# Optimization experiments

Hardware: AMD Instinct MI355X
Metric: run time of the kernel (lower is better)

Reference implementation:

```python
import jax, jax.numpy as jnp
import numpy as np

N_ATOMS = 50000
N_EDGES = 800000
EMB = 128      # emb_size_atom
EMB_BF = 128   # emb_size_bf
N_HIDDEN = 3
INV_SQRT2 = 0.7071067811865476
SILU_SCALE = 1.0 / 0.6  # GemNet ScaledSiLU


def scaled_silu(x):
    return jax.nn.silu(x) * SILU_SCALE


def residual_layer(x, w0, w1):
    # ResidualLayer(units, nLayers=2): two bias-free Dense+ScaledSiLU, then inv_sqrt(2)*(x + y)
    y = scaled_silu(x @ w0)
    y = scaled_silu(y @ w1)
    return (x + y) * INV_SQRT2


def setup_inputs() -> dict:
    key = jax.random.key(0)
    ks = jax.random.split(key, 9)
    s_emb = 1.0 / np.float32(np.sqrt(EMB))
    s_bf = 1.0 / np.float32(np.sqrt(EMB_BF))
    return {
        "h": jax.random.normal(ks[0], (N_ATOMS, EMB), jnp.float32),
        "bf": jax.random.uniform(ks[1], (N_EDGES, EMB_BF), jnp.float32),
        "idx_s": jax.random.randint(ks[2], (N_EDGES,), 0, N_ATOMS, jnp.int64),
        "idx_t": jax.random.randint(ks[3], (N_EDGES,), 0, N_ATOMS, jnp.int64),
        "w_bf": jax.random.normal(ks[4], (EMB_BF, EMB), jnp.float32) * s_bf,
        "w_pre": jax.random.normal(ks[5], (2, EMB, EMB), jnp.float32) * s_emb,
        "w_mlp1": jax.random.normal(ks[6], (EMB, EMB), jnp.float32) * s_emb,
        "w_res": jax.random.normal(ks[7], (N_HIDDEN, 2, EMB, EMB), jnp.float32) * s_emb,
        "scale_sum": jnp.ones((1,), jnp.float32),  # ScalingFactor (1.0 without scale_file)
    }


def reference(h, bf, idx_s, idx_t, w_bf, w_pre, w_mlp1, w_res, scale_sum):
    # pre_residual
    h_res = residual_layer(h, w_pre[0], w_pre[1])          # (nAtoms, EMB)
    # dense_bf: bias-free linear, no activation
    mlp_bf = bf @ w_bf                                     # (nEdges, EMB)
    # gather source embeddings, Hadamard multiply with edge features
    x = h_res[idx_s] * mlp_bf                              # (nEdges, EMB)
    # scatter-sum over target atoms
    x2 = jax.ops.segment_sum(x, idx_t, num_segments=N_ATOMS)  # (nAtoms, EMB)
    x = x2 * scale_sum[0]
    # MLP: Dense+activation, then nHidden residual blocks
    x = scaled_silu(x @ w_mlp1)
    for i in range(N_HIDDEN):
        x = residual_layer(x, w_res[i, 0], w_res[i, 1])
    return x
```

## Files before the change

kernel.cpp:

```cpp
#include <hip/hip_runtime.h>

#define EMB 128
#define NATOMS 50000
#define NEDGES 800000
#define PADN 50176

typedef __attribute__((ext_vector_type(8))) short bf16x8;
typedef __attribute__((ext_vector_type(4))) float f32x4;

static const size_t H_RES_OFF  = 0;
static const size_t X2_OFF     = (size_t)NATOMS * EMB * 4;
static const size_t W_OFF      = 2 * (size_t)NATOMS * EMB * 4;
static const size_t FLAG_OFF   = W_OFF + 10 * 128 * 128 * 2;
static const size_t COUNTS_OFF = (FLAG_OFF + 4 + 255) & ~(size_t)255;
static const size_t SEG_OFF    = COUNTS_OFF + (size_t)PADN * 4;
static const size_t CURSOR_OFF = SEG_OFF + (size_t)PADN * 4;
static const size_t BSUM_OFF   = CURSOR_OFF + (size_t)PADN * 4;
static const size_t ORDER_OFF  = BSUM_OFF + 1024;

__device__ __forceinline__ short f2bf(float f) {
  unsigned u = __float_as_uint(f);
  u += 0x7fffu + ((u >> 16) & 1u);
  return (short)(u >> 16);
}

__device__ __forceinline__ float ssilu(float x) {
  return x * (1.0f / 0.6f) / (1.0f + __expf(-x));
}

__device__ __forceinline__ int xidx(int row, int k) {
  return (row << 7) + ((((k >> 2) ^ (row & 7)) << 2) | (k & 3));
}
__device__ __forceinline__ int bidx(int row, int k) {
  return (row << 7) + ((((k >> 3) ^ (row & 7)) << 3) | (k & 7));
}

__device__ __forceinline__ void stage_w(const short* __restrict__ src, short* dst) {
  const int wave = threadIdx.x >> 6;
  const int lane = threadIdx.x & 63;
  const char* s = (const char*)src;
  char* d = (char*)dst;
#pragma unroll
  for (int i = 0; i < 8; ++i) {
    const int off = wave * 8192 + i * 1024;
    __builtin_amdgcn_global_load_lds(
        (const __attribute__((address_space(1))) void*)(s + off + lane * 16),
        (__attribute__((address_space(3))) void*)(d + off), 16, 0, 0);
  }
}

__device__ __forceinline__ void stage_x(const float* __restrict__ src, int row0, float* x) {
#pragma unroll
  for (int i = 0; i < 8; ++i) {
    const int c = threadIdx.x + i * 256;
    const int row = c >> 5, unit = c & 31;
    f32x4 v = {0.f, 0.f, 0.f, 0.f};
    if (row0 + row < NATOMS) v = *(const f32x4*)(src + (size_t)(row0 + row) * EMB + unit * 4);
    *(f32x4*)&x[(row << 7) + ((unit ^ (row & 7)) << 2)] = v;
  }
}

template <bool SRC_BF16>
__device__ __forceinline__ void gemm_stage(const float* xsrc, const short* ysrc,
                                           const short* w, int wr0, int lr, int lh,
                                           f32x4* acc) {
#pragma unroll
  for (int kk = 0; kk < 4; ++kk) {
    const int k0 = kk * 32 + lh * 8;
    const int ra = wr0 + lr;
    bf16x8 a;
    if constexpr (SRC_BF16) {
      a = *(const bf16x8*)&ysrc[bidx(ra, k0)];
    } else {
      f32x4 u0 = *(const f32x4*)&xsrc[xidx(ra, k0)];
      f32x4 u1 = *(const f32x4*)&xsrc[xidx(ra, k0 + 4)];
      a[0] = f2bf(u0[0]); a[1] = f2bf(u0[1]); a[2] = f2bf(u0[2]); a[3] = f2bf(u0[3]);
      a[4] = f2bf(u1[0]); a[5] = f2bf(u1[1]); a[6] = f2bf(u1[2]); a[7] = f2bf(u1[3]);
    }
#pragma unroll
    for (int j0 = 0; j0 < 8; ++j0) {
      bf16x8 b = *(const bf16x8*)&w[bidx(j0 * 16 + lr, k0)];
      acc[j0] = __builtin_amdgcn_mfma_f32_16x16x32_bf16(a, b, acc[j0], 0, 0, 0);
    }
  }
}

__global__ void prep_weights(const float* __restrict__ wbf, const float* __restrict__ wpre,
                             const float* __restrict__ wmlp1, const float* __restrict__ wres,
                             short* __restrict__ W) {
  const int s = blockIdx.x >> 7;
  const int k = blockIdx.x & 127;
  const int n = threadIdx.x;
  const float* src;
  if (s == 0) src = wbf;
  else if (s <= 2) src = wpre + (s - 1) * 16384;
  else if (s == 3) src = wmlp1;
  else src = wres + (s - 4) * 16384;
  const float v = src[k * EMB + n];
  W[s * 16384 + (n << 7) + ((((k >> 3) ^ (n & 7)) << 3) | (k & 7))] = f2bf(v);
}

__global__ void detect_idx(const int* __restrict__ idx, int* __restrict__ flag) {
  const int lane = threadIdx.x & 63;
  const int v = idx[2 * lane + 1];
  const unsigned long long nz = __ballot(v != 0);
  if (lane == 0) *flag = (nz == 0ull) ? 1 : 0;
}

__device__ __forceinline__ int load_idx(const void* p, int e, int f64) {
  return f64 ? (int)((const long long*)p)[e] : ((const int*)p)[e];
}

__global__ void hist_kernel(const void* __restrict__ idx_t_p, int* __restrict__ counts,
                            const int* __restrict__ flag) {
  const int e = blockIdx.x * 256 + threadIdx.x;
  if (e < NEDGES) atomicAdd(&counts[load_idx(idx_t_p, e, *flag)], 1);
}

__global__ void scan_blocks(const int* __restrict__ counts, int* __restrict__ seg,
                            int* __restrict__ bsum) {
  const int i = blockIdx.x * 256 + threadIdx.x;
  const int lane = threadIdx.x & 63, wave = threadIdx.x >> 6;
  const int v = counts[i];
  int incl = v;
#pragma unroll
  for (int d = 1; d < 64; d <<= 1) {
    int t = __shfl_up(incl, d, 64);
    if (lane >= d) incl += t;
  }
  __shared__ int wtot[4];
  if (lane == 63) wtot[wave] = incl;
  __syncthreads();
  int woff = 0;
  for (int w = 0; w < wave; ++w) woff += wtot[w];
  seg[i] = woff + incl - v;
  if (threadIdx.x == 255) bsum[blockIdx.x] = woff + incl;
}

__global__ void scan_top(int* __restrict__ bsum) {
  const int i = threadIdx.x;
  const int lane = i & 63, wave = i >> 6;
  const int v = (i < 196) ? bsum[i] : 0;
  int incl = v;
#pragma unroll
  for (int d = 1; d < 64; d <<= 1) {
    int t = __shfl_up(incl, d, 64);
    if (lane >= d) incl += t;
  }
  __shared__ int wtot[4];
  if (lane == 63) wtot[wave] = incl;
  __syncthreads();
  int woff = 0;
  for (int w = 0; w < wave; ++w) woff += wtot[w];
  if (i < 196) bsum[i] = woff + incl - v;
}

__global__ void add_off(int* __restrict__ seg, const int* __restrict__ bsum,
                        int* __restrict__ cursor) {
  const int i = blockIdx.x * 256 + threadIdx.x;
  const int s = seg[i] + bsum[blockIdx.x];
  seg[i] = s;
  cursor[i] = s;
}

__global__ void scatter_kernel(const void* __restrict__ idx_t_p, int* __restrict__ cursor,
                               int* __restrict__ order, const int* __restrict__ flag) {
  const int e = blockIdx.x * 256 + threadIdx.x;
  if (e < NEDGES) {
    const int t = load_idx(idx_t_p, e, *flag);
    const int pos = atomicAdd(&cursor[t], 1);
    order[pos] = e;
  }
}

__global__ __launch_bounds__(256, 2) void atom_pre(const float* __restrict__ h,
                                                   float* __restrict__ h_res,
                                                   const short* __restrict__ W) {
  __shared__ float x_lds[64 * 128];
  __shared__ short y_lds[64 * 128];
  __shared__ short w_lds[128 * 128];
  const int lane = threadIdx.x & 63, wave = threadIdx.x >> 6;
  const int lr = lane & 15, lh = lane >> 4;
  const int row0 = blockIdx.x * 64, wr0 = wave * 16;
  const f32x4 vzero = {0.f, 0.f, 0.f, 0.f};

  stage_x(h, row0, x_lds);
  stage_w(W + 1 * 16384, w_lds);
  __syncthreads();

  f32x4 acc[8];
#pragma unroll
  for (int j = 0; j < 8; ++j) acc[j] = vzero;
  gemm_stage<false>(x_lds, nullptr, w_lds, wr0, lr, lh, acc);
#pragma unroll
  for (int j0 = 0; j0 < 8; ++j0)
#pragma unroll
    for (int j = 0; j < 4; ++j)
      y_lds[bidx(wr0 + lh * 4 + j, j0 * 16 + lr)] = f2bf(ssilu(acc[j0][j]));

  __syncthreads();
  stage_w(W + 2 * 16384, w_lds);
  __syncthreads();

#pragma unroll
  for (int j = 0; j < 8; ++j) acc[j] = vzero;
  gemm_stage<true>(nullptr, y_lds, w_lds, wr0, lr, lh, acc);

#pragma unroll
  for (int j = 0; j < 4; ++j) {
    const int row = wr0 + lh * 4 + j;
    const int ga = row0 + row;
    if (ga < NATOMS) {
#pragma unroll
      for (int j0 = 0; j0 < 8; ++j0) {
        const int col = j0 * 16 + lr;
        h_res[(size_t)ga * EMB + col] =
            (x_lds[xidx(row, col)] + ssilu(acc[j0][j])) * 0.70710678118654752440f;
      }
    }
  }
}

__global__ __launch_bounds__(256, 4) void edge_sorted(const float* __restrict__ bf,
                                                      const float* __restrict__ h_res,
                                                      const void* __restrict__ idx_s_p,
                                                      const void* __restrict__ idx_t_p,
                                                      const int* __restrict__ seg,
                                                      const int* __restrict__ order,
                                                      const short* __restrict__ W,
                                                      float* __restrict__ x2,
                                                      const int* __restrict__ flag) {
  __shared__ short w_lds[128 * 128];
  const int lane = threadIdx.x & 63, wave = threadIdx.x >> 6;
  const int lr = lane & 15, lh = lane >> 4;
  const int f64 = *flag;

  stage_w(W, w_lds);
  __syncthreads();

  const int p0 = blockIdx.x * 128 + wave * 32;
  const int r32 = lane & 31;
  const int e_mine = order[p0 + r32];
  const int is_mine = load_idx(idx_s_p, e_mine, f64);
  const int it_mine = load_idx(idx_t_p, e_mine, f64);

  const int e_rf0 = __shfl(e_mine, lr, 64);
  const int e_rf1 = __shfl(e_mine, 16 + lr, 64);

  bf16x8 a_all[2][4];
#pragma unroll
  for (int kk = 0; kk < 4; ++kk) {
#pragma unroll
    for (int rf = 0; rf < 2; ++rf) {
      const int e = rf ? e_rf1 : e_rf0;
      const float* p = bf + (size_t)e * EMB + kk * 32 + lh * 8;
      f32x4 u0 = *(const f32x4*)p;
      f32x4 u1 = *(const f32x4*)(p + 4);
      bf16x8 a;
      a[0] = f2bf(u0[0]); a[1] = f2bf(u0[1]); a[2] = f2bf(u0[2]); a[3] = f2bf(u0[3]);
      a[4] = f2bf(u1[0]); a[5] = f2bf(u1[1]); a[6] = f2bf(u1[2]); a[7] = f2bf(u1[3]);
      a_all[rf][kk] = a;
    }
  }

  f32x4 acc[2][8];
  const f32x4 vzero = {0.f, 0.f, 0.f, 0.f};
#pragma unroll
  for (int rf = 0; rf < 2; ++rf)
#pragma unroll
    for (int j0 = 0; j0 < 8; ++j0) acc[rf][j0] = vzero;

#pragma unroll
  for (int kk = 0; kk < 4; ++kk) {
#pragma unroll
    for (int j0 = 0; j0 < 8; ++j0) {
      bf16x8 b = *(const bf16x8*)&w_lds[bidx(j0 * 16 + lr, kk * 32 + lh * 8)];
      acc[0][j0] = __builtin_amdgcn_mfma_f32_16x16x32_bf16(a_all[0][kk], b, acc[0][j0], 0, 0, 0);
      acc[1][j0] = __builtin_amdgcn_mfma_f32_16x16x32_bf16(a_all[1][kk], b, acc[1][j0], 0, 0, 0);
    }
  }

#pragma unroll
  for (int rf = 0; rf < 2; ++rf) {
#pragma unroll
    for (int j = 0; j < 4; ++j) {
      const int isj = __shfl(is_mine, rf * 16 + 4 * lh + j, 64);
      const float* hrow = h_res + (size_t)isj * EMB;
#pragma unroll
      for (int j0 = 0; j0 < 8; ++j0)
        acc[rf][j0][j] *= hrow[j0 * 16 + lr];
    }
  }

  int r = 0;
  while (r < 32) {
    const int t = __shfl(it_mine, r, 64);
    const unsigned long long bal = __ballot(it_mine == t);
    const unsigned long long m = (bal & 0xffffffffull) >> r;
    const int cnt = (int)__builtin_ctzll(~m);
    const int end = r + cnt;

    float psum[8] = {0.f, 0.f, 0.f, 0.f, 0.f, 0.f, 0.f, 0.f};
#pragma unroll
    for (int rf = 0; rf < 2; ++rf) {
#pragma unroll
      for (int j = 0; j < 4; ++j) {
        const int row = rf * 16 + 4 * lh + j;
        if (row >= r && row < end) {
#pragma unroll
          for (int j0 = 0; j0 < 8; ++j0) psum[j0] += acc[rf][j0][j];
        }
      }
    }
#pragma unroll
    for (int j0 = 0; j0 < 8; ++j0) {
      psum[j0] += __shfl_xor(psum[j0], 16, 64);
      psum[j0] += __shfl_xor(psum[j0], 32, 64);
    }

    const int s0 = seg[t], s1 = seg[t + 1];
    const bool interior = (s0 == p0 + r) && (s1 == p0 + end);
    if (lane < 16) {
      float* orow = x2 + (size_t)t * EMB;
      if (interior) {
#pragma unroll
        for (int j0 = 0; j0 < 8; ++j0) orow[j0 * 16 + lane] = psum[j0];
      } else {
#pragma unroll
        for (int j0 = 0; j0 < 8; ++j0) atomicAdd(&orow[j0 * 16 + lane], psum[j0]);
      }
    }
    r = end;
  }
}

__global__ __launch_bounds__(256, 2) void atom_post(const float* __restrict__ x2,
                                                    float* __restrict__ out,
                                                    const short* __restrict__ W,
                                                    const float* __restrict__ scale_sum) {
  __shared__ float x_lds[64 * 128];
  __shared__ short y_lds[64 * 128];
  __shared__ short w_lds[128 * 128];
  const int lane = threadIdx.x & 63, wave = threadIdx.x >> 6;
  const int lr = lane & 15, lh = lane >> 4;
  const int row0 = blockIdx.x * 64, wr0 = wave * 16;
  const float sc = scale_sum[0];
  const f32x4 vzero = {0.f, 0.f, 0.f, 0.f};

  stage_x(x2, row0, x_lds);
  stage_w(W + 3 * 16384, w_lds);
  __syncthreads();

  f32x4 acc[8];
#pragma unroll
  for (int j = 0; j < 8; ++j) acc[j] = vzero;
  gemm_stage<false>(x_lds, nullptr, w_lds, wr0, lr, lh, acc);
#pragma unroll
  for (int j0 = 0; j0 < 8; ++j0)
#pragma unroll
    for (int j = 0; j < 4; ++j)
      x_lds[xidx(wr0 + lh * 4 + j, j0 * 16 + lr)] = ssilu(acc[j0][j] * sc);

  for (int L = 0; L < 3; ++L) {
    __syncthreads();
    stage_w(W + (size_t)(4 + 2 * L) * 16384, w_lds);
    __syncthreads();
#pragma unroll
    for (int j = 0; j < 8; ++j) acc[j] = vzero;
    gemm_stage<false>(x_lds, nullptr, w_lds, wr0, lr, lh, acc);
#pragma unroll
    for (int j0 = 0; j0 < 8; ++j0)
#pragma unroll
      for (int j = 0; j < 4; ++j)
        y_lds[bidx(wr0 + lh * 4 + j, j0 * 16 + lr)] = f2bf(ssilu(acc[j0][j]));

    __syncthreads();
    stage_w(W + (size_t)(5 + 2 * L) * 16384, w_lds);
    __syncthreads();
#pragma unroll
    for (int j = 0; j < 8; ++j) acc[j] = vzero;
    gemm_stage<true>(nullptr, y_lds, w_lds, wr0, lr, lh, acc);

    if (L < 2) {
#pragma unroll
      for (int j = 0; j < 4; ++j) {
        const int row = wr0 + lh * 4 + j;
#pragma unroll
        for (int j0 = 0; j0 < 8; ++j0) {
          const int col = j0 * 16 + lr;
          const float xv = x_lds[xidx(row, col)];
          x_lds[xidx(row, col)] = (xv + ssilu(acc[j0][j])) * 0.70710678118654752440f;
        }
      }
    } else {
#pragma unroll
      for (int j = 0; j < 4; ++j) {
        const int row = wr0 + lh * 4 + j;
        const int ga = row0 + row;
        if (ga < NATOMS) {
#pragma unroll
          for (int j0 = 0; j0 < 8; ++j0) {
            const int col = j0 * 16 + lr;
            out[(size_t)ga * EMB + col] =
                (x_lds[xidx(row, col)] + ssilu(acc[j0][j])) * 0.70710678118654752440f;
          }
        }
      }
    }
  }
}

extern "C" void kernel_launch(void* const* d_in, const int* in_sizes, int n_in,
                              void* d_out, int out_size, void* d_ws, size_t ws_size,
                              hipStream_t stream) {
  const float* h      = (const float*)d_in[0];
  const float* bf     = (const float*)d_in[1];
  const void*  idx_s  = d_in[2];
  const void*  idx_t  = d_in[3];
  const float* w_bf   = (const float*)d_in[4];
  const float* w_pre  = (const float*)d_in[5];
  const float* w_mlp1 = (const float*)d_in[6];
  const float* w_res  = (const float*)d_in[7];
  const float* scale  = (const float*)d_in[8];
  float* out = (float*)d_out;

  char* ws = (char*)d_ws;
  float* h_res  = (float*)(ws + H_RES_OFF);
  float* x2     = (float*)(ws + X2_OFF);
  short* W      = (short*)(ws + W_OFF);
  int*   flag   = (int*)(ws + FLAG_OFF);
  int*   counts = (int*)(ws + COUNTS_OFF);
  int*   segp   = (int*)(ws + SEG_OFF);
  int*   cursor = (int*)(ws + CURSOR_OFF);
  int*   bsum   = (int*)(ws + BSUM_OFF);
  int*   order  = (int*)(ws + ORDER_OFF);

  hipMemsetAsync(counts, 0, (size_t)PADN * 4, stream);
  hipMemsetAsync(x2, 0, (size_t)NATOMS * EMB * 4, stream);
  prep_weights<<<dim3(10 * 128), dim3(128), 0, stream>>>(w_bf, w_pre, w_mlp1, w_res, W);
  detect_idx<<<dim3(1), dim3(64), 0, stream>>>((const int*)idx_s, flag);

  hist_kernel<<<dim3(NEDGES / 256), dim3(256), 0, stream>>>(idx_t, counts, flag);
  scan_blocks<<<dim3(PADN / 256), dim3(256), 0, stream>>>(counts, segp, bsum);
  scan_top<<<dim3(1), dim3(256), 0, stream>>>(bsum);
  add_off<<<dim3(PADN / 256), dim3(256), 0, stream>>>(segp, bsum, cursor);
  scatter_kernel<<<dim3(NEDGES / 256), dim3(256), 0, stream>>>(idx_t, cursor, order, flag);

  atom_pre<<<dim3((NATOMS + 63) / 64), dim3(256), 0, stream>>>(h, h_res, W);
  edge_sorted<<<dim3(NEDGES / 128), dim3(256), 0, stream>>>(bf, h_res, idx_s, idx_t, segp,
                                                            order, W, x2, flag);
  atom_post<<<dim3((NATOMS + 63) / 64), dim3(256), 0, stream>>>(x2, out, W, scale);
}
```

Before: 356.3 us.

## Swap MFMA operands so edges map to columns; fuse workspace zeroing into kernel

The edge kernel now passes the weight tile as the A operand and the edge features as the B operand. Each lane therefore holds four consecutive output channels of one edge, so the h_res gather becomes a single 16-byte vector load per block and the interior stores are vectorized. The segment reduction now needs a 4-step shuffle butterfly across 16 lanes on 32 values, instead of 2 shuffles on 8, which adds shuffle work and register pressure. The two memsets are replaced with one custom zeroing kernel.

```diff
diff --git a/kernel.cpp b/kernel.cpp
--- a/kernel.cpp
+++ b/kernel.cpp
@@ -100,6 +100,17 @@
   W[s * 16384 + (n << 7) + ((((k >> 3) ^ (n & 7)) << 3) | (k & 7))] = f2bf(v);
 }
 
+__global__ void zero_ws(float* __restrict__ x2, float* __restrict__ counts) {
+  const f32x4 z = {0.f, 0.f, 0.f, 0.f};
+  const int stride = gridDim.x * 256;
+  const int nx = NATOMS * EMB / 4;
+  for (int v = blockIdx.x * 256 + threadIdx.x; v < nx; v += stride)
+    *(f32x4*)(x2 + 4 * (size_t)v) = z;
+  const int nc = PADN / 4;
+  for (int v = blockIdx.x * 256 + threadIdx.x; v < nc; v += stride)
+    *(f32x4*)(counts + 4 * (size_t)v) = z;
+}
+
 __global__ void detect_idx(const int* __restrict__ idx, int* __restrict__ flag) {
   const int lane = threadIdx.x & 63;
   const int v = idx[2 * lane + 1];
@@ -221,15 +232,15 @@
   }
 }
 
-__global__ __launch_bounds__(256, 4) void edge_sorted(const float* __restrict__ bf,
-                                                      const float* __restrict__ h_res,
-                                                      const void* __restrict__ idx_s_p,
-                                                      const void* __restrict__ idx_t_p,
-                                                      const int* __restrict__ seg,
-                                                      const int* __restrict__ order,
-                                                      const short* __restrict__ W,
-                                                      float* __restrict__ x2,
-                                                      const int* __restrict__ flag) {
+__global__ __launch_bounds__(256, 4) void edge_swapped(const float* __restrict__ bf,
+                                                       const float* __restrict__ h_res,
+                                                       const void* __restrict__ idx_s_p,
+                                                       const void* __restrict__ idx_t_p,
+                                                       const int* __restrict__ seg,
+                                                       const int* __restrict__ order,
+                                                       const short* __restrict__ W,
+                                                       float* __restrict__ x2,
+                                                       const int* __restrict__ flag) {
   __shared__ short w_lds[128 * 128];
   const int lane = threadIdx.x & 63, wave = threadIdx.x >> 6;
   const int lr = lane & 15, lh = lane >> 4;
@@ -244,22 +255,24 @@
   const int is_mine = load_idx(idx_s_p, e_mine, f64);
   const int it_mine = load_idx(idx_t_p, e_mine, f64);
 
-  const int e_rf0 = __shfl(e_mine, lr, 64);
-  const int e_rf1 = __shfl(e_mine, 16 + lr, 64);
-
-  bf16x8 a_all[2][4];
+  const int eB0 = __shfl(e_mine, lr, 64);
+  const int eB1 = __shfl(e_mine, 16 + lr, 64);
+  const int isE0 = __shfl(is_mine, lr, 64);
+  const int isE1 = __shfl(is_mine, 16 + lr, 64);
+
+  bf16x8 b_all[2][4];
 #pragma unroll
   for (int kk = 0; kk < 4; ++kk) {
 #pragma unroll
     for (int rf = 0; rf < 2; ++rf) {
-      const int e = rf ? e_rf1 : e_rf0;
+      const int e = rf ? eB1 : eB0;
       const float* p = bf + (size_t)e * EMB + kk * 32 + lh * 8;
       f32x4 u0 = *(const f32x4*)p;
       f32x4 u1 = *(const f32x4*)(p + 4);
-      bf16x8 a;
-      a[0] = f2bf(u0[0]); a[1] = f2bf(u0[1]); a[2] = f2bf(u0[2]); a[3] = f2bf(u0[3]);
-      a[4] = f2bf(u1[0]); a[5] = f2bf(u1[1]); a[6] = f2bf(u1[2]); a[7] = f2bf(u1[3]);
-      a_all[rf][kk] = a;
+      bf16x8 b;
+      b[0] = f2bf(u0[0]); b[1] = f2bf(u0[1]); b[2] = f2bf(u0[2]); b[3] = f2bf(u0[3]);
+      b[4] = f2bf(u1[0]); b[5] = f2bf(u1[1]); b[6] = f2bf(u1[2]); b[7] = f2bf(u1[3]);
+      b_all[rf][kk] = b;
     }
   }
 
@@ -274,21 +287,20 @@
   for (int kk = 0; kk < 4; ++kk) {
 #pragma unroll
     for (int j0 = 0; j0 < 8; ++j0) {
-      bf16x8 b = *(const bf16x8*)&w_lds[bidx(j0 * 16 + lr, kk * 32 + lh * 8)];
-      acc[0][j0] = __builtin_amdgcn_mfma_f32_16x16x32_bf16(a_all[0][kk], b, acc[0][j0], 0, 0, 0);
-      acc[1][j0] = __builtin_amdgcn_mfma_f32_16x16x32_bf16(a_all[1][kk], b, acc[1][j0], 0, 0, 0);
+      bf16x8 a = *(const bf16x8*)&w_lds[bidx(j0 * 16 + lr, kk * 32 + lh * 8)];
+      acc[0][j0] = __builtin_amdgcn_mfma_f32_16x16x32_bf16(a, b_all[0][kk], acc[0][j0], 0, 0, 0);
+      acc[1][j0] = __builtin_amdgcn_mfma_f32_16x16x32_bf16(a, b_all[1][kk], acc[1][j0], 0, 0, 0);
     }
   }
 
 #pragma unroll
   for (int rf = 0; rf < 2; ++rf) {
-#pragma unroll
-    for (int j = 0; j < 4; ++j) {
-      const int isj = __shfl(is_mine, rf * 16 + 4 * lh + j, 64);
-      const float* hrow = h_res + (size_t)isj * EMB;
-#pragma unroll
-      for (int j0 = 0; j0 < 8; ++j0)
-        acc[rf][j0][j] *= hrow[j0 * 16 + lr];
+    const float* hrow = h_res + (size_t)(rf ? isE1 : isE0) * EMB + 4 * lh;
+#pragma unroll
+    for (int j0 = 0; j0 < 8; ++j0) {
+      f32x4 hv = *(const f32x4*)(hrow + 16 * j0);
+#pragma unroll
+      for (int j = 0; j < 4; ++j) acc[rf][j0][j] *= hv[j];
     }
   }
 
@@ -300,34 +312,42 @@
     const int cnt = (int)__builtin_ctzll(~m);
     const int end = r + cnt;
 
-    float psum[8] = {0.f, 0.f, 0.f, 0.f, 0.f, 0.f, 0.f, 0.f};
-#pragma unroll
-    for (int rf = 0; rf < 2; ++rf) {
+    float v[8][4];
+    const bool in0 = (lr >= r) && (lr < end);
+    const bool in1 = (lr + 16 >= r) && (lr + 16 < end);
+#pragma unroll
+    for (int j0 = 0; j0 < 8; ++j0)
 #pragma unroll
       for (int j = 0; j < 4; ++j) {
-        const int row = rf * 16 + 4 * lh + j;
-        if (row >= r && row < end) {
-#pragma unroll
-          for (int j0 = 0; j0 < 8; ++j0) psum[j0] += acc[rf][j0][j];
-        }
+        float s = 0.f;
+        if (in0) s += acc[0][j0][j];
+        if (in1) s += acc[1][j0][j];
+        v[j0][j] = s;
       }
-    }
-#pragma unroll
-    for (int j0 = 0; j0 < 8; ++j0) {
-      psum[j0] += __shfl_xor(psum[j0], 16, 64);
-      psum[j0] += __shfl_xor(psum[j0], 32, 64);
-    }
+#pragma unroll
+    for (int d = 1; d < 16; d <<= 1)
+#pragma unroll
+      for (int j0 = 0; j0 < 8; ++j0)
+#pragma unroll
+        for (int j = 0; j < 4; ++j)
+          v[j0][j] += __shfl_xor(v[j0][j], d, 64);
 
     const int s0 = seg[t], s1 = seg[t + 1];
     const bool interior = (s0 == p0 + r) && (s1 == p0 + end);
-    if (lane < 16) {
-      float* orow = x2 + (size_t)t * EMB;
+    if (lr == 0) {
+      float* orow = x2 + (size_t)t * EMB + 4 * lh;
       if (interior) {
 #pragma unroll
-        for (int j0 = 0; j0 < 8; ++j0) orow[j0 * 16 + lane] = psum[j0];
+        for (int j0 = 0; j0 < 8; ++j0) {
+          f32x4 o = {v[j0][0], v[j0][1], v[j0][2], v[j0][3]};
+          *(f32x4*)(orow + 16 * j0) = o;
+        }
       } else {
 #pragma unroll
-        for (int j0 = 0; j0 < 8; ++j0) atomicAdd(&orow[j0 * 16 + lane], psum[j0]);
+        for (int j0 = 0; j0 < 8; ++j0)
+#pragma unroll
+          for (int j = 0; j < 4; ++j)
+            atomicAdd(&orow[16 * j0 + j], v[j0][j]);
       }
     }
     r = end;
@@ -435,8 +455,7 @@
   int*   bsum   = (int*)(ws + BSUM_OFF);
   int*   order  = (int*)(ws + ORDER_OFF);
 
-  hipMemsetAsync(counts, 0, (size_t)PADN * 4, stream);
-  hipMemsetAsync(x2, 0, (size_t)NATOMS * EMB * 4, stream);
+  zero_ws<<<dim3(1024), dim3(256), 0, stream>>>(x2, (float*)counts);
   prep_weights<<<dim3(10 * 128), dim3(128), 0, stream>>>(w_bf, w_pre, w_mlp1, w_res, W);
   detect_idx<<<dim3(1), dim3(64), 0, stream>>>((const int*)idx_s, flag);
 
@@ -447,7 +466,7 @@
   scatter_kernel<<<dim3(NEDGES / 256), dim3(256), 0, stream>>>(idx_t, cursor, order, flag);
 
   atom_pre<<<dim3((NATOMS + 63) / 64), dim3(256), 0, stream>>>(h, h_res, W);
-  edge_sorted<<<dim3(NEDGES / 128), dim3(256), 0, stream>>>(bf, h_res, idx_s, idx_t, segp,
-                                                            order, W, x2, flag);
+  edge_swapped<<<dim3(NEDGES / 128), dim3(256), 0, stream>>>(bf, h_res, idx_s, idx_t, segp,
+                                                             order, W, x2, flag);
   atom_post<<<dim3((NATOMS + 63) / 64), dim3(256), 0, stream>>>(x2, out, W, scale);
 }
```

After: 462.2 us. 29.7% more time.
